# Kernel tuning notes

Hardware: AMD Instinct MI355X
Metric: run time of the kernel (lower is better)

## Reference

```python
import jax, jax.numpy as jnp
import numpy as np

N, E = 10000, 320000
IN_D, HID, OUT_D, EIN, KH = 128, 32, 128, 1, 32
BN_EPS = 1e-5  # torch BatchNorm1d default eps


def bn(x, g, b):
    # training-mode batch norm with biased variance (torch normalization semantics)
    m = jnp.mean(x, axis=0)
    v = jnp.mean((x - m) ** 2, axis=0)
    return g * (x - m) / jnp.sqrt(v + BN_EPS) + b


def setup_inputs() -> dict:
    key = jax.random.key(0)
    ks = jax.random.split(key, 8)

    def w(k, shape, s=0.05):
        return jax.random.normal(k, shape, dtype=jnp.float32) * s

    return {
        "H": jax.random.normal(ks[0], (N, IN_D), dtype=jnp.float32),
        "edge_attr": jax.random.normal(ks[1], (E, EIN), dtype=jnp.float32),
        "edges": jax.random.randint(ks[2], (2, E), 0, N),
        # linear1: input_dim -> hidden_dim
        "w1": w(ks[3], (HID, IN_D)), "b1": jnp.zeros((HID,), jnp.float32),
        # kernel MLP: edge_input_dim -> kernel_hidden -> (hidden+1)*hidden
        "kw1": w(ks[4], (KH, EIN)), "kb1": jnp.zeros((KH,), jnp.float32),
        "kw2": w(ks[5], ((HID + 1) * HID, KH)), "kb2": jnp.zeros(((HID + 1) * HID,), jnp.float32),
        # linear2: hidden -> output
        "w2": w(ks[6], (OUT_D, HID)), "b2": jnp.zeros((OUT_D,), jnp.float32),
        # batchnorm affine params
        "g_in": jnp.ones((IN_D,), jnp.float32), "beta_in": jnp.zeros((IN_D,), jnp.float32),
        "g_msg": jnp.ones((HID,), jnp.float32), "beta_msg": jnp.zeros((HID,), jnp.float32),
        "g_upd": jnp.ones((HID,), jnp.float32), "beta_upd": jnp.zeros((HID,), jnp.float32),
        "g_out": jnp.ones((OUT_D,), jnp.float32), "beta_out": jnp.zeros((OUT_D,), jnp.float32),
    }


def reference(H, edge_attr, edges, w1, b1, kw1, kb1, kw2, kb2, w2, b2,
              g_in, beta_in, g_msg, beta_msg, g_upd, beta_upd, g_out, beta_out):
    node_out, node_in = edges[0], edges[1]

    Hn = bn(H, g_in, beta_in)                    # input_batch_norm
    layer_input = jax.nn.relu(Hn)                # dropout -> identity (eval)

    # message: gather -> linear1 -> BN -> relu
    msg = layer_input[node_in] @ w1.T + b1       # [E, HID]
    msg = jax.nn.relu(bn(msg, g_msg, beta_msg))

    # edge-conditioned dynamic kernel: [E, HID+1, HID]
    kern = jax.nn.relu(edge_attr @ kw1.T + kb1) @ kw2.T + kb2
    kern = kern.reshape(E, HID + 1, HID)
    # per-edge matvec + per-edge bias row
    msg = jnp.einsum('ejk,ek->ej', kern[:, 1:, :], msg) + kern[:, 0, :]

    # aggregate: scatter_add into nodes
    upd = jax.ops.segment_sum(msg, node_out, num_segments=N)
    upd = jax.nn.relu(bn(upd, g_upd, beta_upd))

    out = upd @ w2.T + b2                        # linear2
    return bn(out, g_out, beta_out)              # output_batch_norm
```

## Files before the change

kernel.cpp:

```cpp
#include <hip/hip_runtime.h>
#include <math.h>

constexpr int N_    = 10000;
constexpr int E_    = 320000;
constexpr int IND   = 128;
constexpr int HID   = 32;
constexpr int OUTD  = 128;
constexpr int NIV   = 33;
constexpr float EPS = 1e-5f;

constexpr size_t OFF_SUMH   = 0;
constexpr size_t OFF_SQH    = 128;
constexpr size_t OFF_SUMP   = 256;
constexpr size_t OFF_SQP    = 288;
constexpr size_t OFF_SUMU   = 320;
constexpr size_t OFF_SQU    = 352;
constexpr size_t OFF_SUMO   = 384;
constexpr size_t OFF_SQO    = 512;
constexpr size_t OFF_OCC    = 640;
constexpr size_t OFF_DEGIN  = 704;
constexpr size_t OFF_DEGOUT = 10704;
constexpr size_t ZERO_CNT   = 20704;
constexpr size_t OFF_STARTS = 20740;
constexpr size_t OFF_CUR    = 30744;
constexpr size_t OFF_C1     = 40744;
constexpr size_t OFF_C0     = 75592;
constexpr size_t OFF_P      = 110440;
constexpr size_t OFF_UPD    = 430440;
constexpr size_t OFF_AEN    = 750440;

__device__ inline int compute_bps(const float* kw1, const float* kb1, float* bp) {
    int m = 0;
    for (int k = 0; k < 32; ++k) {
        float w = kw1[k];
        if (w != 0.f) bp[m++] = -kb1[k] / w;
    }
    for (int a = 1; a < m; ++a) {
        float v = bp[a]; int b = a - 1;
        while (b >= 0 && bp[b] > v) { bp[b+1] = bp[b]; --b; }
        bp[b+1] = v;
    }
    return m;
}

__global__ __launch_bounds__(256)
void k_A(const float* __restrict__ H,
         const float* __restrict__ ea, const int* __restrict__ edges,
         const float* __restrict__ kw1, const float* __restrict__ kb1,
         const float* __restrict__ kw2, const float* __restrict__ kb2,
         float* __restrict__ ws) {
    __shared__ float sel1[32], sel0[32];
    __shared__ float shS[256], shQ[256];
    __shared__ int locc[NIV];
    __shared__ float bps[32];
    int* wsi = (int*)ws;
    int t = threadIdx.x;
    int bid = blockIdx.x;

    if (bid < 33) {
        int i = bid;
        if (t == 0) {
            float bp[32];
            int m = compute_bps(kw1, kb1, bp);
            float arep;
            if (m == 0 || i > m) arep = 0.f;
            else if (i == 0)     arep = bp[0]   - (1.f + 0.5f*fabsf(bp[0]));
            else if (i == m)     arep = bp[m-1] + (1.f + 0.5f*fabsf(bp[m-1]));
            else                 arep = (bp[i-1] < bp[i]) ? 0.5f*(bp[i-1] + bp[i]) : bp[i-1];
            for (int k = 0; k < 32; ++k) {
                bool s = (arep * kw1[k] + kb1[k]) > 0.f;
                sel1[k] = s ? kw1[k] : 0.f;
                sel0[k] = s ? kb1[k] : 0.f;
            }
        }
        __syncthreads();
        for (int r = t; r < 1056; r += 256) {
            float a1 = 0.f, a0 = 0.f;
            for (int k = 0; k < 32; ++k) {
                float w = kw2[r*32 + k];
                a1 += w * sel1[k];
                a0 += w * sel0[k];
            }
            ws[OFF_C1 + (size_t)i*1056 + r] = a1;
            ws[OFF_C0 + (size_t)i*1056 + r] = a0 + kb2[r];
        }
    } else if (bid < 161) {
        int b2 = bid - 33;
        int col = t & 127, half = t >> 7;
        float s = 0.f, q = 0.f;
        for (int r = b2*2 + half; r < N_; r += 128*2) {
            float x = H[(size_t)r*IND + col];
            s += x; q += x*x;
        }
        shS[t] = s; shQ[t] = q;
        __syncthreads();
        if (t < 128) {
            atomicAdd(&ws[OFF_SUMH + t], shS[t] + shS[t+128]);
            atomicAdd(&ws[OFF_SQH  + t], shQ[t] + shQ[t+128]);
        }
    } else {
        int b2 = bid - 161;
        if (t < NIV) locc[t] = 0;
        if (t == 0) {
            float bp[32];
            int m = compute_bps(kw1, kb1, bp);
            for (int k = 0; k < 32; ++k) bps[k] = (k < m) ? bp[k] : 3.0e38f;
        }
        __syncthreads();
        for (int e = b2*256 + t; e < E_; e += 313*256) {
            float a = ea[e];
            int cnt = 0;
            #pragma unroll
            for (int k = 0; k < 32; ++k) cnt += (bps[k] < a) ? 1 : 0;
            atomicAdd(&locc[cnt], 1);
            atomicAdd(&wsi[OFF_DEGIN  + edges[E_ + e]], 1);
            atomicAdd(&wsi[OFF_DEGOUT + edges[e]],      1);
        }
        __syncthreads();
        if (t < NIV && locc[t] > 0) atomicAdd(&wsi[OFF_OCC + t], locc[t]);
    }
}

__global__ __launch_bounds__(256)
void k_B(const float* __restrict__ H, const float* __restrict__ w1,
         const float* __restrict__ b1, const float* __restrict__ g_in,
         const float* __restrict__ beta_in, float* __restrict__ ws) {
    __shared__ float w1L[32*129];
    __shared__ float xl[8][128];
    __shared__ int part[256];
    int* wsi = (int*)ws;
    int t = threadIdx.x;

    if (blockIdx.x == 0) {
        int base = t * 40;
        int loc[40];
        int s = 0;
        for (int i = 0; i < 40; ++i) {
            int idx = base + i;
            int v = (idx < N_) ? wsi[OFF_DEGOUT + idx] : 0;
            loc[i] = s; s += v;
        }
        part[t] = s;
        __syncthreads();
        for (int off = 1; off < 256; off <<= 1) {
            int add = (t >= off) ? part[t - off] : 0;
            __syncthreads();
            part[t] += add;
            __syncthreads();
        }
        int pre = (t > 0) ? part[t-1] : 0;
        for (int i = 0; i < 40; ++i) {
            int idx = base + i;
            if (idx <= N_) {
                int v = pre + loc[i];
                wsi[OFF_STARTS + idx] = v;
                if (idx < N_) wsi[OFF_CUR + idx] = v;
            }
        }
        return;
    }

    int g = t >> 5, j = t & 31;
    for (int idx = t; idx < 4096; idx += 256)
        w1L[(idx >> 7)*129 + (idx & 127)] = w1[idx];

    int n = (blockIdx.x - 1)*8 + g;
    float4 h4 = ((const float4*)(H + (size_t)n*IND))[j];
    float4 m4 = ((const float4*)(ws + OFF_SUMH))[j];
    float4 q4 = ((const float4*)(ws + OFF_SQH))[j];
    float4 gg = ((const float4*)g_in)[j];
    float4 bb = ((const float4*)beta_in)[j];
    float4 xv;
    {
        float* hp = (float*)&h4; float* mp = (float*)&m4; float* qp = (float*)&q4;
        float* gp = (float*)&gg; float* bp = (float*)&bb; float* xp = (float*)&xv;
        for (int i = 0; i < 4; ++i) {
            float mean = mp[i] * (1.f/N_);
            float var  = qp[i] * (1.f/N_) - mean*mean;
            float istd = 1.f / sqrtf(var + EPS);
            float gc = gp[i]*istd, bc = bp[i] - mean*gc;
            xp[i] = fmaxf(fmaf(gc, hp[i], bc), 0.f);
        }
    }
    ((float4*)&xl[g][0])[j] = xv;
    __syncthreads();
    float p = b1[j];
    const float* wr = &w1L[j*129];
    const float* xr = &xl[g][0];
    #pragma unroll 8
    for (int k = 0; k < 128; ++k) p = fmaf(wr[k], xr[k], p);
    ws[OFF_P + (size_t)n*HID + j] = p;
}

__global__ __launch_bounds__(256)
void k_C(const float* __restrict__ ea, const int* __restrict__ edges,
         const float* __restrict__ kw1, const float* __restrict__ kb1,
         float* __restrict__ ws) {
    __shared__ float shS[256], shQ[256];
    __shared__ float bps[32];
    int* wsi = (int*)ws;
    int t = threadIdx.x;
    if (blockIdx.x < 313) {
        if (t == 0) {
            float bp[32];
            int m = compute_bps(kw1, kb1, bp);
            for (int k = 0; k < 32; ++k) bps[k] = (k < m) ? bp[k] : 3.0e38f;
        }
        __syncthreads();
        float2* aen = (float2*)(ws + OFF_AEN);
        int b2 = blockIdx.x;
        for (int e = b2*256 + t; e < E_; e += 313*256) {
            int   nout = edges[e];
            int   nin  = edges[E_ + e];
            float a    = ea[e];
            int iv = 0;
            #pragma unroll
            for (int k = 0; k < 32; ++k) iv += (bps[k] < a) ? 1 : 0;
            int pos = atomicAdd(&wsi[OFF_CUR + nout], 1);
            float2 rec; rec.x = a; rec.y = __int_as_float(nin | (iv << 16));
            aen[pos] = rec;
        }
    } else {
        int b2 = blockIdx.x - 313;
        int j = t & 31, cp = t >> 5;
        float s = 0.f, q = 0.f;
        for (int n = b2*8 + cp; n < N_; n += 64*8) {
            float w = (float)wsi[OFF_DEGIN + n];
            float p = ws[OFF_P + (size_t)n*HID + j];
            s += w*p; q += w*p*p;
        }
        shS[t] = s; shQ[t] = q;
        __syncthreads();
        if (t < 32) {
            float S = 0.f, Qq = 0.f;
            for (int c = 0; c < 8; ++c) { S += shS[t + 32*c]; Qq += shQ[t + 32*c]; }
            atomicAdd(&ws[OFF_SUMP + t], S);
            atomicAdd(&ws[OFF_SQP  + t], Qq);
        }
    }
}

__global__ __launch_bounds__(256)
void k_D(const float* __restrict__ g_msg, const float* __restrict__ beta_msg,
         float* __restrict__ ws) {
    __shared__ float A[4][32*33];
    __shared__ float Bv[4][32];
    __shared__ float zl[8][4][32];
    __shared__ float shS[256], shQ[256];
    __shared__ int s_slot0, s_slot1;
    int* wsi = (int*)ws;
    int t = threadIdx.x, g = t >> 5, j = t & 31;

    if (t == 0) {
        int a0 = -1, a1 = -1;
        for (int i = 0; i < NIV; ++i)
            if (wsi[OFF_OCC + i] > 0) { if (a0 < 0) a0 = i; else if (a1 < 0) a1 = i; }
        s_slot0 = a0; s_slot1 = a1;
    }
    __syncthreads();
    int s0 = s_slot0, s1 = s_slot1;

    for (int idx = t; idx < 1024; idx += 256) {
        int jj = idx >> 5, kk = idx & 31;
        A[0][jj*33+kk] = (s0 >= 0) ? ws[OFF_C1 + (size_t)s0*1056 + 32 + idx] : 0.f;
        A[1][jj*33+kk] = (s0 >= 0) ? ws[OFF_C0 + (size_t)s0*1056 + 32 + idx] : 0.f;
        A[2][jj*33+kk] = (s1 >= 0) ? ws[OFF_C1 + (size_t)s1*1056 + 32 + idx] : 0.f;
        A[3][jj*33+kk] = (s1 >= 0) ? ws[OFF_C0 + (size_t)s1*1056 + 32 + idx] : 0.f;
    }
    if (t < 32) {
        Bv[0][t] = (s0 >= 0) ? ws[OFF_C1 + (size_t)s0*1056 + t] : 0.f;
        Bv[1][t] = (s0 >= 0) ? ws[OFF_C0 + (size_t)s0*1056 + t] : 0.f;
        Bv[2][t] = (s1 >= 0) ? ws[OFF_C1 + (size_t)s1*1056 + t] : 0.f;
        Bv[3][t] = (s1 >= 0) ? ws[OFF_C0 + (size_t)s1*1056 + t] : 0.f;
    }
    float mP = ws[OFF_SUMP + j] * (1.f/E_);
    float vP = ws[OFF_SQP  + j] * (1.f/E_) - mP*mP;
    float istd = 1.f / sqrtf(vP + EPS);
    float gc = g_msg[j]*istd, bc = beta_msg[j] - mP*gc;
    __syncthreads();

    int n = blockIdx.x*8 + g;
    int st = wsi[OFF_STARTS + n], en = wsi[OFF_STARTS + n + 1];
    float za0 = 0.f, zb0 = 0.f, za1 = 0.f, zb1 = 0.f;
    float suma0 = 0.f, suma1 = 0.f, c0f = 0.f, c1f = 0.f, rfall = 0.f;
    const float2* aen = (const float2*)(ws + OFF_AEN);

    for (int base = st; base < en; base += 32) {
        int cnt = en - base; if (cnt > 32) cnt = 32;
        float a_j = 0.f; int meta_j = 0;
        if (j < cnt) {
            float2 r = aen[base + j];
            a_j = r.x; meta_j = __float_as_int(r.y);
        }
        for (int k = 0; k < cnt; k += 4) {
            float pv[4], aa[4]; int ivv[4]; bool val[4];
            #pragma unroll
            for (int u = 0; u < 4; ++u) {
                int kk = (k + u) & 31;
                aa[u]  = __shfl(a_j, kk, 32);
                int mt = __shfl(meta_j, kk, 32);
                val[u] = (k + u) < cnt;
                int nin = mt & 0xFFFF; ivv[u] = mt >> 16;
                pv[u] = ws[OFF_P + (size_t)nin*HID + j];
            }
            #pragma unroll
            for (int u = 0; u < 4; ++u) {
                if (!val[u]) continue;
                float q = fmaxf(fmaf(gc, pv[u], bc), 0.f);
                float a = aa[u]; int iv = ivv[u];
                if (iv == s0)      { za0 = fmaf(a, q, za0); zb0 += q; suma0 += a; c0f += 1.f; }
                else if (iv == s1) { za1 = fmaf(a, q, za1); zb1 += q; suma1 += a; c1f += 1.f; }
                else {
                    const float* C1r = ws + OFF_C1 + (size_t)iv*1056;
                    const float* C0r = ws + OFF_C0 + (size_t)iv*1056;
                    float d1 = 0.f, d0 = 0.f;
                    for (int k2 = 0; k2 < 32; ++k2) {
                        float qk = __shfl(q, k2, 32);
                        d1 += C1r[32 + j*32 + k2] * qk;
                        d0 += C0r[32 + j*32 + k2] * qk;
                    }
                    rfall += a*(d1 + C1r[j]) + (d0 + C0r[j]);
                }
            }
        }
    }
    zl[g][0][j] = za0; zl[g][1][j] = zb0; zl[g][2][j] = za1; zl[g][3][j] = zb1;
    __syncthreads();

    float acc = rfall;
    if (s0 >= 0) acc += suma0*Bv[0][j] + c0f*Bv[1][j];
    if (s1 >= 0) acc += suma1*Bv[2][j] + c1f*Bv[3][j];
    const float* z0 = zl[g][0]; const float* z1 = zl[g][1];
    const float* z2 = zl[g][2]; const float* z3 = zl[g][3];
    #pragma unroll 4
    for (int k = 0; k < 32; ++k) {
        acc += A[0][j*33+k]*z0[k] + A[1][j*33+k]*z1[k]
             + A[2][j*33+k]*z2[k] + A[3][j*33+k]*z3[k];
    }
    ws[OFF_UPD + (size_t)n*HID + j] = acc;

    shS[t] = acc; shQ[t] = acc*acc;
    __syncthreads();
    if (t < 32) {
        float S = 0.f, Qq = 0.f;
        for (int c = 0; c < 8; ++c) { S += shS[t + 32*c]; Qq += shQ[t + 32*c]; }
        atomicAdd(&ws[OFF_SUMU + t], S);
        atomicAdd(&ws[OFF_SQU  + t], Qq);
    }
}

__global__ __launch_bounds__(256)
void k_F(const float* __restrict__ w2, const float* __restrict__ b2,
         const float* __restrict__ g_upd, const float* __restrict__ beta_upd,
         float* __restrict__ ws, float* __restrict__ out) {
    __shared__ float U[2][HID];
    __shared__ float shS[256], shQ[256];
    int t = threadIdx.x, nh = t >> 7, o = t & 127;
    float gc = 0.f, bc = 0.f;
    if (o < 32) {
        float m = ws[OFF_SUMU + o]*(1.f/N_);
        float v = ws[OFF_SQU  + o]*(1.f/N_) - m*m;
        float istd = 1.f/sqrtf(v + EPS);
        gc = g_upd[o]*istd; bc = beta_upd[o] - m*gc;
    }
    float w2r[32];
    for (int k = 0; k < 32; ++k) w2r[k] = w2[o*32 + k];
    float bo = b2[o];
    float sO = 0.f, qO = 0.f;
    for (int base = blockIdx.x*2; base < N_; base += gridDim.x*2) {
        int n = base + nh;
        if (o < 32) {
            float u = ws[OFF_UPD + (size_t)n*HID + o];
            U[nh][o] = fmaxf(fmaf(gc, u, bc), 0.f);
        }
        __syncthreads();
        float v = bo;
        for (int k = 0; k < 32; ++k) v = fmaf(w2r[k], U[nh][k], v);
        out[(size_t)n*OUTD + o] = v;
        sO += v; qO += v*v;
        __syncthreads();
    }
    shS[t] = sO; shQ[t] = qO;
    __syncthreads();
    if (t < 128) {
        atomicAdd(&ws[OFF_SUMO + t], shS[t] + shS[t+128]);
        atomicAdd(&ws[OFF_SQO  + t], shQ[t] + shQ[t+128]);
    }
}

__global__ __launch_bounds__(256)
void k_G(const float* __restrict__ g_out, const float* __restrict__ beta_out,
         const float* __restrict__ ws, float* __restrict__ out) {
    int g = blockIdx.x*blockDim.x + threadIdx.x;
    if (g >= N_*OUTD) return;
    int o = g & 127;
    float m = ws[OFF_SUMO + o]*(1.f/N_);
    float v = ws[OFF_SQO  + o]*(1.f/N_) - m*m;
    float istd = 1.f/sqrtf(v + EPS);
    out[g] = g_out[o]*istd*(out[g] - m) + beta_out[o];
}

extern "C" void kernel_launch(void* const* d_in, const int* in_sizes, int n_in,
                              void* d_out, int out_size, void* d_ws, size_t ws_size,
                              hipStream_t stream) {
    const float* H        = (const float*)d_in[0];
    const float* ea       = (const float*)d_in[1];
    const int*   edges    = (const int*)  d_in[2];
    const float* w1       = (const float*)d_in[3];
    const float* b1       = (const float*)d_in[4];
    const float* kw1      = (const float*)d_in[5];
    const float* kb1      = (const float*)d_in[6];
    const float* kw2      = (const float*)d_in[7];
    const float* kb2      = (const float*)d_in[8];
    const float* w2       = (const float*)d_in[9];
    const float* b2       = (const float*)d_in[10];
    const float* g_in     = (const float*)d_in[11];
    const float* beta_in  = (const float*)d_in[12];
    const float* g_msg    = (const float*)d_in[13];
    const float* beta_msg = (const float*)d_in[14];
    const float* g_upd    = (const float*)d_in[15];
    const float* beta_upd = (const float*)d_in[16];
    const float* g_out    = (const float*)d_in[17];
    const float* beta_out = (const float*)d_in[18];
    float* ws  = (float*)d_ws;
    float* out = (float*)d_out;

    hipMemsetAsync(d_ws, 0, ZERO_CNT*sizeof(float), stream);
    hipLaunchKernelGGL(k_A, dim3(474),  dim3(256), 0, stream, H, ea, edges, kw1, kb1, kw2, kb2, ws);
    hipLaunchKernelGGL(k_B, dim3(1251), dim3(256), 0, stream, H, w1, b1, g_in, beta_in, ws);
    hipLaunchKernelGGL(k_C, dim3(377),  dim3(256), 0, stream, ea, edges, kw1, kb1, ws);
    hipLaunchKernelGGL(k_D, dim3(1250), dim3(256), 0, stream, g_msg, beta_msg, ws);
    hipLaunchKernelGGL(k_F, dim3(250),  dim3(256), 0, stream, w2, b2, g_upd, beta_upd, ws, out);
    hipLaunchKernelGGL(k_G, dim3((N_*OUTD + 255)/256), dim3(256), 0, stream, g_out, beta_out, ws, out);
}
```

Measured before the change: 257.9 us.

## Map one node per wavefront in k_D with prefetched edge records

The aggregation kernel now gives each destination node a full 64-lane wavefront (4 nodes per block, twice the grid) instead of a 32-lane half-wave. Each lane loads the edge records itself, and the next 8 records are prefetched into registers while the current 8 are processed. Accumulation into the two dominant kernel slots becomes branchless masked FMAs, and the rare fallback path passes the q vector through shared memory instead of shuffles. This is meant to remove divergence between the two nodes that used to share a wave and to hide edge-record load latency. The cost is that the upper 32 lanes redo the lower half's work, so twice as many threads are used.

```diff
diff --git a/kernel.cpp b/kernel.cpp
--- a/kernel.cpp
+++ b/kernel.cpp
@@ -245,11 +245,15 @@
          float* __restrict__ ws) {
     __shared__ float A[4][32*33];
     __shared__ float Bv[4][32];
-    __shared__ float zl[8][4][32];
+    __shared__ float zx[4][4][32];
+    __shared__ float fb[4][32];
     __shared__ float shS[256], shQ[256];
     __shared__ int s_slot0, s_slot1;
     int* wsi = (int*)ws;
-    int t = threadIdx.x, g = t >> 5, j = t & 31;
+    int t = threadIdx.x;
+    int w = t >> 6;
+    int lane = t & 63;
+    int j = lane & 31;
 
     if (t == 0) {
         int a0 = -1, a1 = -1;
@@ -279,67 +283,81 @@
     float gc = g_msg[j]*istd, bc = beta_msg[j] - mP*gc;
     __syncthreads();
 
-    int n = blockIdx.x*8 + g;
+    int n = blockIdx.x*4 + w;
     int st = wsi[OFF_STARTS + n], en = wsi[OFF_STARTS + n + 1];
     float za0 = 0.f, zb0 = 0.f, za1 = 0.f, zb1 = 0.f;
     float suma0 = 0.f, suma1 = 0.f, c0f = 0.f, c1f = 0.f, rfall = 0.f;
     const float2* aen = (const float2*)(ws + OFF_AEN);
 
-    for (int base = st; base < en; base += 32) {
-        int cnt = en - base; if (cnt > 32) cnt = 32;
-        float a_j = 0.f; int meta_j = 0;
-        if (j < cnt) {
-            float2 r = aen[base + j];
-            a_j = r.x; meta_j = __float_as_int(r.y);
-        }
-        for (int k = 0; k < cnt; k += 4) {
-            float pv[4], aa[4]; int ivv[4]; bool val[4];
-            #pragma unroll
-            for (int u = 0; u < 4; ++u) {
-                int kk = (k + u) & 31;
-                aa[u]  = __shfl(a_j, kk, 32);
-                int mt = __shfl(meta_j, kk, 32);
-                val[u] = (k + u) < cnt;
-                int nin = mt & 0xFFFF; ivv[u] = mt >> 16;
-                pv[u] = ws[OFF_P + (size_t)nin*HID + j];
+    if (st < en) {
+        float2 rcur[8], rnext[8];
+        #pragma unroll
+        for (int q = 0; q < 8; ++q) {
+            int idx = st + q; if (idx >= en) idx = en - 1;
+            rcur[q] = aen[idx];
+        }
+        for (int base = st; base < en; base += 8) {
+            int nb = base + 8;
+            if (nb < en) {
+                #pragma unroll
+                for (int q = 0; q < 8; ++q) {
+                    int idx = nb + q; if (idx >= en) idx = en - 1;
+                    rnext[q] = aen[idx];
+                }
             }
             #pragma unroll
-            for (int u = 0; u < 4; ++u) {
-                if (!val[u]) continue;
-                float q = fmaxf(fmaf(gc, pv[u], bc), 0.f);
-                float a = aa[u]; int iv = ivv[u];
-                if (iv == s0)      { za0 = fmaf(a, q, za0); zb0 += q; suma0 += a; c0f += 1.f; }
-                else if (iv == s1) { za1 = fmaf(a, q, za1); zb1 += q; suma1 += a; c1f += 1.f; }
-                else {
+            for (int q = 0; q < 8; ++q) {
+                bool valid = (base + q) < en;
+                float a = rcur[q].x;
+                int  mt = __float_as_int(rcur[q].y);
+                int nin = mt & 0xFFFF, iv = mt >> 16;
+                float pv = ws[OFF_P + (size_t)nin*HID + j];
+                float qv = fmaxf(fmaf(gc, pv, bc), 0.f);
+                if (__builtin_expect(valid && iv != s0 && iv != s1, 0)) {
+                    if (lane < 32) fb[w][j] = qv;
                     const float* C1r = ws + OFF_C1 + (size_t)iv*1056;
                     const float* C0r = ws + OFF_C0 + (size_t)iv*1056;
                     float d1 = 0.f, d0 = 0.f;
                     for (int k2 = 0; k2 < 32; ++k2) {
-                        float qk = __shfl(q, k2, 32);
+                        float qk = fb[w][k2];
                         d1 += C1r[32 + j*32 + k2] * qk;
                         d0 += C0r[32 + j*32 + k2] * qk;
                     }
                     rfall += a*(d1 + C1r[j]) + (d0 + C0r[j]);
+                } else {
+                    float w0 = (valid && iv == s0) ? 1.f : 0.f;
+                    float w1 = (valid && iv == s1) ? 1.f : 0.f;
+                    float w0a = w0 * a, w1a = w1 * a;
+                    za0 = fmaf(w0a, qv, za0); zb0 = fmaf(w0, qv, zb0);
+                    za1 = fmaf(w1a, qv, za1); zb1 = fmaf(w1, qv, zb1);
+                    suma0 += w0a; c0f += w0;
+                    suma1 += w1a; c1f += w1;
                 }
             }
-        }
-    }
-    zl[g][0][j] = za0; zl[g][1][j] = zb0; zl[g][2][j] = za1; zl[g][3][j] = zb1;
+            #pragma unroll
+            for (int q = 0; q < 8; ++q) rcur[q] = rnext[q];
+        }
+    }
+
+    if (lane < 32) {
+        zx[w][0][j] = za0; zx[w][1][j] = zb0; zx[w][2][j] = za1; zx[w][3][j] = zb1;
+    }
     __syncthreads();
 
     float acc = rfall;
     if (s0 >= 0) acc += suma0*Bv[0][j] + c0f*Bv[1][j];
     if (s1 >= 0) acc += suma1*Bv[2][j] + c1f*Bv[3][j];
-    const float* z0 = zl[g][0]; const float* z1 = zl[g][1];
-    const float* z2 = zl[g][2]; const float* z3 = zl[g][3];
+    const float* z0 = zx[w][0]; const float* z1 = zx[w][1];
+    const float* z2 = zx[w][2]; const float* z3 = zx[w][3];
     #pragma unroll 4
     for (int k = 0; k < 32; ++k) {
         acc += A[0][j*33+k]*z0[k] + A[1][j*33+k]*z1[k]
              + A[2][j*33+k]*z2[k] + A[3][j*33+k]*z3[k];
     }
-    ws[OFF_UPD + (size_t)n*HID + j] = acc;
-
-    shS[t] = acc; shQ[t] = acc*acc;
+    if (lane < 32) ws[OFF_UPD + (size_t)n*HID + j] = acc;
+
+    shS[t] = (lane < 32) ? acc : 0.f;
+    shQ[t] = (lane < 32) ? acc*acc : 0.f;
     __syncthreads();
     if (t < 32) {
         float S = 0.f, Qq = 0.f;
@@ -429,7 +447,7 @@
     hipLaunchKernelGGL(k_A, dim3(474),  dim3(256), 0, stream, H, ea, edges, kw1, kb1, kw2, kb2, ws);
     hipLaunchKernelGGL(k_B, dim3(1251), dim3(256), 0, stream, H, w1, b1, g_in, beta_in, ws);
     hipLaunchKernelGGL(k_C, dim3(377),  dim3(256), 0, stream, ea, edges, kw1, kb1, ws);
-    hipLaunchKernelGGL(k_D, dim3(1250), dim3(256), 0, stream, g_msg, beta_msg, ws);
+    hipLaunchKernelGGL(k_D, dim3(2500), dim3(256), 0, stream, g_msg, beta_msg, ws);
     hipLaunchKernelGGL(k_F, dim3(250),  dim3(256), 0, stream, w2, b2, g_upd, beta_upd, ws, out);
     hipLaunchKernelGGL(k_G, dim3((N_*OUTD + 255)/256), dim3(256), 0, stream, g_out, beta_out, ws, out);
 }
```

Result: slower. 300.8 us (+16.6%).

## Fuse all stages into one cooperative persistent kernel with grid syncs

Applied to the files above, without the earlier changes.

Replaces the memset plus six kernel launches with a single cooperative kernel. It runs at most 512 persistent blocks and separates the stages with grid.sync, removing the per-launch gaps and drain bubbles between dependent kernels. The edge-aggregation inner loop is also unrolled to 8 and made branch-light by using predicated weights for the two common intervals. The prefix scan now recomputes degrees instead of keeping a per-thread local array. The cost is grid-wide barriers, fewer blocks than some stages previously used, and a fallback to the old multi-kernel path if the cooperative launch fails.

```diff
diff --git a/kernel.cpp b/kernel.cpp
--- a/kernel.cpp
+++ b/kernel.cpp
@@ -1,5 +1,8 @@
 #include <hip/hip_runtime.h>
+#include <hip/hip_cooperative_groups.h>
 #include <math.h>
+
+namespace cg = cooperative_groups;
 
 constexpr int N_    = 10000;
 constexpr int E_    = 320000;
@@ -44,6 +47,375 @@
 }
 
 __global__ __launch_bounds__(256)
+void k_mega(const float* __restrict__ H, const float* __restrict__ ea,
+            const int* __restrict__ edges,
+            const float* __restrict__ w1, const float* __restrict__ b1,
+            const float* __restrict__ kw1, const float* __restrict__ kb1,
+            const float* __restrict__ kw2, const float* __restrict__ kb2,
+            const float* __restrict__ w2, const float* __restrict__ b2,
+            const float* __restrict__ g_in, const float* __restrict__ beta_in,
+            const float* __restrict__ g_msg, const float* __restrict__ beta_msg,
+            const float* __restrict__ g_upd, const float* __restrict__ beta_upd,
+            const float* __restrict__ g_out, const float* __restrict__ beta_out,
+            float* __restrict__ ws, float* __restrict__ out) {
+    cg::grid_group grid = cg::this_grid();
+    __shared__ float S[6144];
+    __shared__ int s_slots[2];
+    int* wsi = (int*)ws;
+    const int t = threadIdx.x;
+    const int bid = blockIdx.x;
+    const int GD  = gridDim.x;
+
+    for (size_t i = (size_t)bid*256 + t; i < ZERO_CNT; i += (size_t)GD*256)
+        ws[i] = 0.f;
+    grid.sync();
+
+    {
+        float* sel1 = S;         float* sel0 = S + 32;
+        float* shS  = S + 64;    float* shQ  = S + 320;
+        int*   locc = (int*)(S + 576);
+        float* bps  = S + 640;
+        for (int task = bid; task < 474; task += GD) {
+            if (task < 33) {
+                int i = task;
+                if (t == 0) {
+                    float bp[32];
+                    int m = compute_bps(kw1, kb1, bp);
+                    float arep;
+                    if (m == 0 || i > m) arep = 0.f;
+                    else if (i == 0)     arep = bp[0]   - (1.f + 0.5f*fabsf(bp[0]));
+                    else if (i == m)     arep = bp[m-1] + (1.f + 0.5f*fabsf(bp[m-1]));
+                    else                 arep = (bp[i-1] < bp[i]) ? 0.5f*(bp[i-1] + bp[i]) : bp[i-1];
+                    for (int k = 0; k < 32; ++k) {
+                        bool s = (arep * kw1[k] + kb1[k]) > 0.f;
+                        sel1[k] = s ? kw1[k] : 0.f;
+                        sel0[k] = s ? kb1[k] : 0.f;
+                    }
+                }
+                __syncthreads();
+                for (int r = t; r < 1056; r += 256) {
+                    float a1 = 0.f, a0 = 0.f;
+                    for (int k = 0; k < 32; ++k) {
+                        float w = kw2[r*32 + k];
+                        a1 += w * sel1[k];
+                        a0 += w * sel0[k];
+                    }
+                    ws[OFF_C1 + (size_t)i*1056 + r] = a1;
+                    ws[OFF_C0 + (size_t)i*1056 + r] = a0 + kb2[r];
+                }
+            } else if (task < 161) {
+                int b2 = task - 33;
+                int col = t & 127, half = t >> 7;
+                float s = 0.f, q = 0.f;
+                for (int r = b2*2 + half; r < N_; r += 128*2) {
+                    float x = H[(size_t)r*IND + col];
+                    s += x; q += x*x;
+                }
+                shS[t] = s; shQ[t] = q;
+                __syncthreads();
+                if (t < 128) {
+                    atomicAdd(&ws[OFF_SUMH + t], shS[t] + shS[t+128]);
+                    atomicAdd(&ws[OFF_SQH  + t], shQ[t] + shQ[t+128]);
+                }
+            } else {
+                int b2 = task - 161;
+                if (t < NIV) locc[t] = 0;
+                if (t == 0) {
+                    float bp[32];
+                    int m = compute_bps(kw1, kb1, bp);
+                    for (int k = 0; k < 32; ++k) bps[k] = (k < m) ? bp[k] : 3.0e38f;
+                }
+                __syncthreads();
+                for (int e = b2*256 + t; e < E_; e += 313*256) {
+                    float a = ea[e];
+                    int cnt = 0;
+                    #pragma unroll
+                    for (int k = 0; k < 32; ++k) cnt += (bps[k] < a) ? 1 : 0;
+                    atomicAdd(&locc[cnt], 1);
+                    atomicAdd(&wsi[OFF_DEGIN  + edges[E_ + e]], 1);
+                    atomicAdd(&wsi[OFF_DEGOUT + edges[e]],      1);
+                }
+                __syncthreads();
+                if (t < NIV && locc[t] > 0) atomicAdd(&wsi[OFF_OCC + t], locc[t]);
+            }
+            __syncthreads();
+        }
+    }
+    grid.sync();
+
+    {
+        float* w1L  = S;
+        float* xl   = S + 4128;
+        int*   part = (int*)(S + 5152);
+        for (int idx = t; idx < 4096; idx += 256)
+            w1L[(idx >> 7)*129 + (idx & 127)] = w1[idx];
+        __syncthreads();
+        for (int task = bid; task < 1251; task += GD) {
+            if (task == 0) {
+                int base = t * 40;
+                int s = 0;
+                for (int i = 0; i < 40; ++i) {
+                    int idx = base + i;
+                    s += (idx < N_) ? wsi[OFF_DEGOUT + idx] : 0;
+                }
+                part[t] = s;
+                __syncthreads();
+                for (int off = 1; off < 256; off <<= 1) {
+                    int add = (t >= off) ? part[t - off] : 0;
+                    __syncthreads();
+                    part[t] += add;
+                    __syncthreads();
+                }
+                int run = (t > 0) ? part[t-1] : 0;
+                for (int i = 0; i < 40; ++i) {
+                    int idx = base + i;
+                    if (idx <= N_) {
+                        wsi[OFF_STARTS + idx] = run;
+                        if (idx < N_) {
+                            wsi[OFF_CUR + idx] = run;
+                            run += wsi[OFF_DEGOUT + idx];
+                        }
+                    }
+                }
+            } else {
+                int g = t >> 5, j = t & 31;
+                int n = (task - 1)*8 + g;
+                float* xlg = xl + g*128;
+                float4 h4 = ((const float4*)(H + (size_t)n*IND))[j];
+                float4 m4 = ((const float4*)(ws + OFF_SUMH))[j];
+                float4 q4 = ((const float4*)(ws + OFF_SQH))[j];
+                float4 gg = ((const float4*)g_in)[j];
+                float4 bb = ((const float4*)beta_in)[j];
+                float4 xv;
+                {
+                    float* hp = (float*)&h4; float* mp = (float*)&m4; float* qp = (float*)&q4;
+                    float* gp = (float*)&gg; float* bp = (float*)&bb; float* xp = (float*)&xv;
+                    for (int i = 0; i < 4; ++i) {
+                        float mean = mp[i] * (1.f/N_);
+                        float var  = qp[i] * (1.f/N_) - mean*mean;
+                        float istd = 1.f / sqrtf(var + EPS);
+                        float gcv = gp[i]*istd, bcv = bp[i] - mean*gcv;
+                        xp[i] = fmaxf(fmaf(gcv, hp[i], bcv), 0.f);
+                    }
+                }
+                ((float4*)xlg)[j] = xv;
+                __syncthreads();
+                float p = b1[j];
+                const float* wr = &w1L[j*129];
+                #pragma unroll 8
+                for (int k = 0; k < 128; ++k) p = fmaf(wr[k], xlg[k], p);
+                ws[OFF_P + (size_t)n*HID + j] = p;
+            }
+            __syncthreads();
+        }
+    }
+    grid.sync();
+
+    {
+        float* bps = S;
+        float* shS = S + 64;  float* shQ = S + 320;
+        for (int task = bid; task < 377; task += GD) {
+            if (task < 313) {
+                if (t == 0) {
+                    float bp[32];
+                    int m = compute_bps(kw1, kb1, bp);
+                    for (int k = 0; k < 32; ++k) bps[k] = (k < m) ? bp[k] : 3.0e38f;
+                }
+                __syncthreads();
+                float2* aen = (float2*)(ws + OFF_AEN);
+                for (int e = task*256 + t; e < E_; e += 313*256) {
+                    int   nout = edges[e];
+                    int   nin  = edges[E_ + e];
+                    float a    = ea[e];
+                    int iv = 0;
+                    #pragma unroll
+                    for (int k = 0; k < 32; ++k) iv += (bps[k] < a) ? 1 : 0;
+                    int pos = atomicAdd(&wsi[OFF_CUR + nout], 1);
+                    float2 rec; rec.x = a; rec.y = __int_as_float(nin | (iv << 16));
+                    aen[pos] = rec;
+                }
+            } else {
+                int b2 = task - 313;
+                int j = t & 31, cp = t >> 5;
+                float s = 0.f, q = 0.f;
+                for (int n = b2*8 + cp; n < N_; n += 64*8) {
+                    float w = (float)wsi[OFF_DEGIN + n];
+                    float p = ws[OFF_P + (size_t)n*HID + j];
+                    s += w*p; q += w*p*p;
+                }
+                shS[t] = s; shQ[t] = q;
+                __syncthreads();
+                if (t < 32) {
+                    float Sm = 0.f, Qq = 0.f;
+                    for (int c = 0; c < 8; ++c) { Sm += shS[t + 32*c]; Qq += shQ[t + 32*c]; }
+                    atomicAdd(&ws[OFF_SUMP + t], Sm);
+                    atomicAdd(&ws[OFF_SQP  + t], Qq);
+                }
+            }
+            __syncthreads();
+        }
+    }
+    grid.sync();
+
+    {
+        float* A   = S;
+        float* Bv  = S + 4224;
+        float* zl  = S + 4352;
+        float* shS = S + 5376;   float* shQ = S + 5632;
+        int g = t >> 5, j = t & 31;
+        if (t == 0) {
+            int a0 = -1, a1 = -1;
+            for (int i = 0; i < NIV; ++i)
+                if (wsi[OFF_OCC + i] > 0) { if (a0 < 0) a0 = i; else if (a1 < 0) a1 = i; }
+            s_slots[0] = a0; s_slots[1] = a1;
+        }
+        __syncthreads();
+        int s0 = s_slots[0], s1 = s_slots[1];
+        for (int idx = t; idx < 1024; idx += 256) {
+            int jj = idx >> 5, kk = idx & 31;
+            A[0*1056 + jj*33+kk] = (s0 >= 0) ? ws[OFF_C1 + (size_t)s0*1056 + 32 + idx] : 0.f;
+            A[1*1056 + jj*33+kk] = (s0 >= 0) ? ws[OFF_C0 + (size_t)s0*1056 + 32 + idx] : 0.f;
+            A[2*1056 + jj*33+kk] = (s1 >= 0) ? ws[OFF_C1 + (size_t)s1*1056 + 32 + idx] : 0.f;
+            A[3*1056 + jj*33+kk] = (s1 >= 0) ? ws[OFF_C0 + (size_t)s1*1056 + 32 + idx] : 0.f;
+        }
+        if (t < 32) {
+            Bv[0*32+t] = (s0 >= 0) ? ws[OFF_C1 + (size_t)s0*1056 + t] : 0.f;
+            Bv[1*32+t] = (s0 >= 0) ? ws[OFF_C0 + (size_t)s0*1056 + t] : 0.f;
+            Bv[2*32+t] = (s1 >= 0) ? ws[OFF_C1 + (size_t)s1*1056 + t] : 0.f;
+            Bv[3*32+t] = (s1 >= 0) ? ws[OFF_C0 + (size_t)s1*1056 + t] : 0.f;
+        }
+        float mP = ws[OFF_SUMP + j] * (1.f/E_);
+        float vP = ws[OFF_SQP  + j] * (1.f/E_) - mP*mP;
+        float istd = 1.f / sqrtf(vP + EPS);
+        float gc = g_msg[j]*istd, bc = beta_msg[j] - mP*gc;
+        __syncthreads();
+
+        float sumS = 0.f, sumQ = 0.f;
+        const float2* aen = (const float2*)(ws + OFF_AEN);
+        for (int task = bid; task < 1250; task += GD) {
+            int n = task*8 + g;
+            int st = wsi[OFF_STARTS + n], en = wsi[OFF_STARTS + n + 1];
+            float za0 = 0.f, zb0 = 0.f, za1 = 0.f, zb1 = 0.f;
+            float suma0 = 0.f, suma1 = 0.f, c0f = 0.f, c1f = 0.f, rfall = 0.f;
+            for (int base = st; base < en; base += 32) {
+                int cnt = en - base; if (cnt > 32) cnt = 32;
+                float a_j = 0.f; int meta_j = 0;
+                if (j < cnt) {
+                    float2 r = aen[base + j];
+                    a_j = r.x; meta_j = __float_as_int(r.y);
+                }
+                for (int k = 0; k < cnt; k += 8) {
+                    float pv[8], aa[8]; int ivv[8]; bool val[8];
+                    #pragma unroll
+                    for (int u = 0; u < 8; ++u) {
+                        int kk = (k + u) & 31;
+                        aa[u]  = __shfl(a_j, kk, 32);
+                        int mt = __shfl(meta_j, kk, 32);
+                        val[u] = (k + u) < cnt;
+                        int nin = mt & 0xFFFF; ivv[u] = mt >> 16;
+                        pv[u] = ws[OFF_P + (size_t)nin*HID + j];
+                    }
+                    #pragma unroll
+                    for (int u = 0; u < 8; ++u) {
+                        float qv = fmaxf(fmaf(gc, pv[u], bc), 0.f);
+                        float a = aa[u]; int iv = ivv[u];
+                        if (__builtin_expect(val[u] && iv != s0 && iv != s1, 0)) {
+                            const float* C1r = ws + OFF_C1 + (size_t)iv*1056;
+                            const float* C0r = ws + OFF_C0 + (size_t)iv*1056;
+                            float d1 = 0.f, d0 = 0.f;
+                            for (int k2 = 0; k2 < 32; ++k2) {
+                                float qk = __shfl(qv, k2, 32);
+                                d1 += C1r[32 + j*32 + k2] * qk;
+                                d0 += C0r[32 + j*32 + k2] * qk;
+                            }
+                            rfall += a*(d1 + C1r[j]) + (d0 + C0r[j]);
+                        } else {
+                            float w0 = (val[u] && iv == s0) ? 1.f : 0.f;
+                            float w1v = (val[u] && iv == s1) ? 1.f : 0.f;
+                            float w0a = w0 * a, w1a = w1v * a;
+                            za0 = fmaf(w0a, qv, za0); zb0 = fmaf(w0, qv, zb0);
+                            za1 = fmaf(w1a, qv, za1); zb1 = fmaf(w1v, qv, zb1);
+                            suma0 += w0a; c0f += w0;
+                            suma1 += w1a; c1f += w1v;
+                        }
+                    }
+                }
+            }
+            zl[(g*4+0)*32+j] = za0; zl[(g*4+1)*32+j] = zb0;
+            zl[(g*4+2)*32+j] = za1; zl[(g*4+3)*32+j] = zb1;
+            __syncthreads();
+            float acc = rfall;
+            if (s0 >= 0) acc += suma0*Bv[0*32+j] + c0f*Bv[1*32+j];
+            if (s1 >= 0) acc += suma1*Bv[2*32+j] + c1f*Bv[3*32+j];
+            const float* z0 = zl + (g*4+0)*32; const float* z1 = zl + (g*4+1)*32;
+            const float* z2 = zl + (g*4+2)*32; const float* z3 = zl + (g*4+3)*32;
+            #pragma unroll 4
+            for (int k = 0; k < 32; ++k) {
+                acc += A[0*1056 + j*33+k]*z0[k] + A[1*1056 + j*33+k]*z1[k]
+                     + A[2*1056 + j*33+k]*z2[k] + A[3*1056 + j*33+k]*z3[k];
+            }
+            ws[OFF_UPD + (size_t)n*HID + j] = acc;
+            sumS += acc; sumQ += acc*acc;
+            __syncthreads();
+        }
+        shS[t] = sumS; shQ[t] = sumQ;
+        __syncthreads();
+        if (t < 32) {
+            float Sm = 0.f, Qq = 0.f;
+            for (int c = 0; c < 8; ++c) { Sm += shS[t + 32*c]; Qq += shQ[t + 32*c]; }
+            atomicAdd(&ws[OFF_SUMU + t], Sm);
+            atomicAdd(&ws[OFF_SQU  + t], Qq);
+        }
+    }
+    grid.sync();
+
+    {
+        float* U   = S;
+        float* shS = S + 64;   float* shQ = S + 320;
+        int nh = t >> 7, o = t & 127;
+        float gc = 0.f, bc = 0.f;
+        if (o < 32) {
+            float m = ws[OFF_SUMU + o]*(1.f/N_);
+            float v = ws[OFF_SQU  + o]*(1.f/N_) - m*m;
+            float istd = 1.f/sqrtf(v + EPS);
+            gc = g_upd[o]*istd; bc = beta_upd[o] - m*gc;
+        }
+        float w2r[32];
+        for (int k = 0; k < 32; ++k) w2r[k] = w2[o*32 + k];
+        float bo = b2[o];
+        float sO = 0.f, qO = 0.f;
+        for (int task = bid; task < 5000; task += GD) {
+            int n = task*2 + nh;
+            if (o < 32) {
+                float u = ws[OFF_UPD + (size_t)n*HID + o];
+                U[nh*32 + o] = fmaxf(fmaf(gc, u, bc), 0.f);
+            }
+            __syncthreads();
+            float v = bo;
+            for (int k = 0; k < 32; ++k) v = fmaf(w2r[k], U[nh*32 + k], v);
+            out[(size_t)n*OUTD + o] = v;
+            sO += v; qO += v*v;
+            __syncthreads();
+        }
+        shS[t] = sO; shQ[t] = qO;
+        __syncthreads();
+        if (t < 128) {
+            atomicAdd(&ws[OFF_SUMO + t], shS[t] + shS[t+128]);
+            atomicAdd(&ws[OFF_SQO  + t], shQ[t] + shQ[t+128]);
+        }
+    }
+    grid.sync();
+
+    for (size_t i = (size_t)bid*256 + t; i < (size_t)N_*OUTD; i += (size_t)GD*256) {
+        int o = (int)(i & 127);
+        float m = ws[OFF_SUMO + o]*(1.f/N_);
+        float v = ws[OFF_SQO  + o]*(1.f/N_) - m*m;
+        float istd = 1.f/sqrtf(v + EPS);
+        out[i] = g_out[o]*istd*(out[i] - m) + beta_out[o];
+    }
+}
+
+__global__ __launch_bounds__(256)
 void k_A(const float* __restrict__ H,
          const float* __restrict__ ea, const int* __restrict__ edges,
          const float* __restrict__ kw1, const float* __restrict__ kb1,
@@ -56,7 +428,6 @@
     int* wsi = (int*)ws;
     int t = threadIdx.x;
     int bid = blockIdx.x;
-
     if (bid < 33) {
         int i = bid;
         if (t == 0) {
@@ -130,15 +501,12 @@
     __shared__ int part[256];
     int* wsi = (int*)ws;
     int t = threadIdx.x;
-
     if (blockIdx.x == 0) {
         int base = t * 40;
-        int loc[40];
         int s = 0;
         for (int i = 0; i < 40; ++i) {
             int idx = base + i;
-            int v = (idx < N_) ? wsi[OFF_DEGOUT + idx] : 0;
-            loc[i] = s; s += v;
+            s += (idx < N_) ? wsi[OFF_DEGOUT + idx] : 0;
         }
         part[t] = s;
         __syncthreads();
@@ -148,22 +516,19 @@
             part[t] += add;
             __syncthreads();
         }
-        int pre = (t > 0) ? part[t-1] : 0;
+        int run = (t > 0) ? part[t-1] : 0;
         for (int i = 0; i < 40; ++i) {
             int idx = base + i;
             if (idx <= N_) {
-                int v = pre + loc[i];
-                wsi[OFF_STARTS + idx] = v;
-                if (idx < N_) wsi[OFF_CUR + idx] = v;
+                wsi[OFF_STARTS + idx] = run;
+                if (idx < N_) { wsi[OFF_CUR + idx] = run; run += wsi[OFF_DEGOUT + idx]; }
             }
         }
         return;
     }
-
     int g = t >> 5, j = t & 31;
     for (int idx = t; idx < 4096; idx += 256)
         w1L[(idx >> 7)*129 + (idx & 127)] = w1[idx];
-
     int n = (blockIdx.x - 1)*8 + g;
     float4 h4 = ((const float4*)(H + (size_t)n*IND))[j];
     float4 m4 = ((const float4*)(ws + OFF_SUMH))[j];
@@ -250,7 +615,6 @@
     __shared__ int s_slot0, s_slot1;
     int* wsi = (int*)ws;
     int t = threadIdx.x, g = t >> 5, j = t & 31;
-
     if (t == 0) {
         int a0 = -1, a1 = -1;
         for (int i = 0; i < NIV; ++i)
@@ -259,7 +623,6 @@
     }
     __syncthreads();
     int s0 = s_slot0, s1 = s_slot1;
-
     for (int idx = t; idx < 1024; idx += 256) {
         int jj = idx >> 5, kk = idx & 31;
         A[0][jj*33+kk] = (s0 >= 0) ? ws[OFF_C1 + (size_t)s0*1056 + 32 + idx] : 0.f;
@@ -278,13 +641,11 @@
     float istd = 1.f / sqrtf(vP + EPS);
     float gc = g_msg[j]*istd, bc = beta_msg[j] - mP*gc;
     __syncthreads();
-
     int n = blockIdx.x*8 + g;
     int st = wsi[OFF_STARTS + n], en = wsi[OFF_STARTS + n + 1];
     float za0 = 0.f, zb0 = 0.f, za1 = 0.f, zb1 = 0.f;
     float suma0 = 0.f, suma1 = 0.f, c0f = 0.f, c1f = 0.f, rfall = 0.f;
     const float2* aen = (const float2*)(ws + OFF_AEN);
-
     for (int base = st; base < en; base += 32) {
         int cnt = en - base; if (cnt > 32) cnt = 32;
         float a_j = 0.f; int meta_j = 0;
@@ -292,10 +653,10 @@
             float2 r = aen[base + j];
             a_j = r.x; meta_j = __float_as_int(r.y);
         }
-        for (int k = 0; k < cnt; k += 4) {
-            float pv[4], aa[4]; int ivv[4]; bool val[4];
+        for (int k = 0; k < cnt; k += 8) {
+            float pv[8], aa[8]; int ivv[8]; bool val[8];
             #pragma unroll
-            for (int u = 0; u < 4; ++u) {
+            for (int u = 0; u < 8; ++u) {
                 int kk = (k + u) & 31;
                 aa[u]  = __shfl(a_j, kk, 32);
                 int mt = __shfl(meta_j, kk, 32);
@@ -304,29 +665,33 @@
                 pv[u] = ws[OFF_P + (size_t)nin*HID + j];
             }
             #pragma unroll
-            for (int u = 0; u < 4; ++u) {
-                if (!val[u]) continue;
-                float q = fmaxf(fmaf(gc, pv[u], bc), 0.f);
+            for (int u = 0; u < 8; ++u) {
+                float qv = fmaxf(fmaf(gc, pv[u], bc), 0.f);
                 float a = aa[u]; int iv = ivv[u];
-                if (iv == s0)      { za0 = fmaf(a, q, za0); zb0 += q; suma0 += a; c0f += 1.f; }
-                else if (iv == s1) { za1 = fmaf(a, q, za1); zb1 += q; suma1 += a; c1f += 1.f; }
-                else {
+                if (__builtin_expect(val[u] && iv != s0 && iv != s1, 0)) {
                     const float* C1r = ws + OFF_C1 + (size_t)iv*1056;
                     const float* C0r = ws + OFF_C0 + (size_t)iv*1056;
                     float d1 = 0.f, d0 = 0.f;
                     for (int k2 = 0; k2 < 32; ++k2) {
-                        float qk = __shfl(q, k2, 32);
+                        float qk = __shfl(qv, k2, 32);
                         d1 += C1r[32 + j*32 + k2] * qk;
                         d0 += C0r[32 + j*32 + k2] * qk;
                     }
                     rfall += a*(d1 + C1r[j]) + (d0 + C0r[j]);
+                } else {
+                    float w0 = (val[u] && iv == s0) ? 1.f : 0.f;
+                    float w1v = (val[u] && iv == s1) ? 1.f : 0.f;
+                    float w0a = w0 * a, w1a = w1v * a;
+                    za0 = fmaf(w0a, qv, za0); zb0 = fmaf(w0, qv, zb0);
+                    za1 = fmaf(w1a, qv, za1); zb1 = fmaf(w1v, qv, zb1);
+                    suma0 += w0a; c0f += w0;
+                    suma1 += w1a; c1f += w1v;
                 }
             }
         }
     }
     zl[g][0][j] = za0; zl[g][1][j] = zb0; zl[g][2][j] = za1; zl[g][3][j] = zb1;
     __syncthreads();
-
     float acc = rfall;
     if (s0 >= 0) acc += suma0*Bv[0][j] + c0f*Bv[1][j];
     if (s1 >= 0) acc += suma1*Bv[2][j] + c1f*Bv[3][j];
@@ -338,7 +703,6 @@
              + A[2][j*33+k]*z2[k] + A[3][j*33+k]*z3[k];
     }
     ws[OFF_UPD + (size_t)n*HID + j] = acc;
-
     shS[t] = acc; shQ[t] = acc*acc;
     __syncthreads();
     if (t < 32) {
@@ -425,11 +789,30 @@
     float* ws  = (float*)d_ws;
     float* out = (float*)d_out;
 
-    hipMemsetAsync(d_ws, 0, ZERO_CNT*sizeof(float), stream);
-    hipLaunchKernelGGL(k_A, dim3(474),  dim3(256), 0, stream, H, ea, edges, kw1, kb1, kw2, kb2, ws);
-    hipLaunchKernelGGL(k_B, dim3(1251), dim3(256), 0, stream, H, w1, b1, g_in, beta_in, ws);
-    hipLaunchKernelGGL(k_C, dim3(377),  dim3(256), 0, stream, ea, edges, kw1, kb1, ws);
-    hipLaunchKernelGGL(k_D, dim3(1250), dim3(256), 0, stream, g_msg, beta_msg, ws);
-    hipLaunchKernelGGL(k_F, dim3(250),  dim3(256), 0, stream, w2, b2, g_upd, beta_upd, ws, out);
-    hipLaunchKernelGGL(k_G, dim3((N_*OUTD + 255)/256), dim3(256), 0, stream, g_out, beta_out, ws, out);
+    int perCU = 0;
+    hipError_t oerr = hipOccupancyMaxActiveBlocksPerMultiprocessor(&perCU, k_mega, 256, 0);
+    int blocks = (oerr == hipSuccess && perCU > 0) ? perCU * 256 : 0;
+    if (blocks > 512) blocks = 512;
+
+    hipError_t lerr = hipErrorUnknown;
+    if (blocks > 0) {
+        void* args[] = {
+            (void*)&H, (void*)&ea, (void*)&edges, (void*)&w1, (void*)&b1,
+            (void*)&kw1, (void*)&kb1, (void*)&kw2, (void*)&kb2,
+            (void*)&w2, (void*)&b2, (void*)&g_in, (void*)&beta_in,
+            (void*)&g_msg, (void*)&beta_msg, (void*)&g_upd, (void*)&beta_upd,
+            (void*)&g_out, (void*)&beta_out, (void*)&ws, (void*)&out
+        };
+        lerr = hipLaunchCooperativeKernel((void*)k_mega, dim3(blocks), dim3(256),
+                                          args, 0, stream);
+    }
+    if (lerr != hipSuccess) {
+        hipMemsetAsync(d_ws, 0, ZERO_CNT*sizeof(float), stream);
+        hipLaunchKernelGGL(k_A, dim3(474),  dim3(256), 0, stream, H, ea, edges, kw1, kb1, kw2, kb2, ws);
+        hipLaunchKernelGGL(k_B, dim3(1251), dim3(256), 0, stream, H, w1, b1, g_in, beta_in, ws);
+        hipLaunchKernelGGL(k_C, dim3(377),  dim3(256), 0, stream, ea, edges, kw1, kb1, ws);
+        hipLaunchKernelGGL(k_D, dim3(1250), dim3(256), 0, stream, g_msg, beta_msg, ws);
+        hipLaunchKernelGGL(k_F, dim3(250),  dim3(256), 0, stream, w2, b2, g_upd, beta_upd, ws, out);
+        hipLaunchKernelGGL(k_G, dim3((N_*OUTD + 255)/256), dim3(256), 0, stream, g_out, beta_out, ws, out);
+    }
 }
```

Measured after the change: 462.6 us. 1.79x slower.

## Flatten k_D edge loop across warps for 20-node blocks with shared-memory atomics

Applied to the files above, without the earlier changes.

k_D now has each block own 20 consecutive destination nodes and spreads all their edges across the 8 warps, instead of one warp walking one node's edge list. The local node index is packed into the edge record; the source index and interval id are repacked into fewer bits. Per-node partial sums are accumulated with LDS float atomics, then finished with float4 reads from a padded coefficient tile. The aim is to even out per-node degree imbalance and raise memory-level parallelism, at the cost of shared atomics and fewer blocks.

```diff
diff --git a/kernel.cpp b/kernel.cpp
--- a/kernel.cpp
+++ b/kernel.cpp
@@ -7,6 +7,7 @@
 constexpr int HID   = 32;
 constexpr int OUTD  = 128;
 constexpr int NIV   = 33;
+constexpr int NPB   = 20;
 constexpr float EPS = 1e-5f;
 
 constexpr size_t OFF_SUMH   = 0;
@@ -216,8 +217,10 @@
             int iv = 0;
             #pragma unroll
             for (int k = 0; k < 32; ++k) iv += (bps[k] < a) ? 1 : 0;
+            int nl = nout % NPB;
             int pos = atomicAdd(&wsi[OFF_CUR + nout], 1);
-            float2 rec; rec.x = a; rec.y = __int_as_float(nin | (iv << 16));
+            float2 rec; rec.x = a;
+            rec.y = __int_as_float(nin | (iv << 14) | (nl << 20));
             aen[pos] = rec;
         }
     } else {
@@ -243,11 +246,13 @@
 __global__ __launch_bounds__(256)
 void k_D(const float* __restrict__ g_msg, const float* __restrict__ beta_msg,
          float* __restrict__ ws) {
-    __shared__ float A[4][32*33];
+    __shared__ __align__(16) float A[4][32*36];
     __shared__ float Bv[4][32];
-    __shared__ float zl[8][4][32];
+    __shared__ __align__(16) float accZ[NPB][4][32];
+    __shared__ float accS[NPB][4];
+    __shared__ float accF[NPB][32];
     __shared__ float shS[256], shQ[256];
-    __shared__ int s_slot0, s_slot1;
+    __shared__ int s_slots[2];
     int* wsi = (int*)ws;
     int t = threadIdx.x, g = t >> 5, j = t & 31;
 
@@ -255,17 +260,20 @@
         int a0 = -1, a1 = -1;
         for (int i = 0; i < NIV; ++i)
             if (wsi[OFF_OCC + i] > 0) { if (a0 < 0) a0 = i; else if (a1 < 0) a1 = i; }
-        s_slot0 = a0; s_slot1 = a1;
-    }
-    __syncthreads();
-    int s0 = s_slot0, s1 = s_slot1;
+        s_slots[0] = a0; s_slots[1] = a1;
+    }
+    for (int idx = t; idx < NPB*4*32; idx += 256) ((float*)accZ)[idx] = 0.f;
+    for (int idx = t; idx < NPB*4;    idx += 256) ((float*)accS)[idx] = 0.f;
+    for (int idx = t; idx < NPB*32;   idx += 256) ((float*)accF)[idx] = 0.f;
+    __syncthreads();
+    int s0 = s_slots[0], s1 = s_slots[1];
 
     for (int idx = t; idx < 1024; idx += 256) {
         int jj = idx >> 5, kk = idx & 31;
-        A[0][jj*33+kk] = (s0 >= 0) ? ws[OFF_C1 + (size_t)s0*1056 + 32 + idx] : 0.f;
-        A[1][jj*33+kk] = (s0 >= 0) ? ws[OFF_C0 + (size_t)s0*1056 + 32 + idx] : 0.f;
-        A[2][jj*33+kk] = (s1 >= 0) ? ws[OFF_C1 + (size_t)s1*1056 + 32 + idx] : 0.f;
-        A[3][jj*33+kk] = (s1 >= 0) ? ws[OFF_C0 + (size_t)s1*1056 + 32 + idx] : 0.f;
+        A[0][jj*36+kk] = (s0 >= 0) ? ws[OFF_C1 + (size_t)s0*1056 + 32 + idx] : 0.f;
+        A[1][jj*36+kk] = (s0 >= 0) ? ws[OFF_C0 + (size_t)s0*1056 + 32 + idx] : 0.f;
+        A[2][jj*36+kk] = (s1 >= 0) ? ws[OFF_C1 + (size_t)s1*1056 + 32 + idx] : 0.f;
+        A[3][jj*36+kk] = (s1 >= 0) ? ws[OFF_C0 + (size_t)s1*1056 + 32 + idx] : 0.f;
     }
     if (t < 32) {
         Bv[0][t] = (s0 >= 0) ? ws[OFF_C1 + (size_t)s0*1056 + t] : 0.f;
@@ -279,67 +287,83 @@
     float gc = g_msg[j]*istd, bc = beta_msg[j] - mP*gc;
     __syncthreads();
 
-    int n = blockIdx.x*8 + g;
-    int st = wsi[OFF_STARTS + n], en = wsi[OFF_STARTS + n + 1];
-    float za0 = 0.f, zb0 = 0.f, za1 = 0.f, zb1 = 0.f;
-    float suma0 = 0.f, suma1 = 0.f, c0f = 0.f, c1f = 0.f, rfall = 0.f;
+    int n0 = blockIdx.x * NPB;
+    int span0 = wsi[OFF_STARTS + n0], span1 = wsi[OFF_STARTS + n0 + NPB];
     const float2* aen = (const float2*)(ws + OFF_AEN);
 
-    for (int base = st; base < en; base += 32) {
-        int cnt = en - base; if (cnt > 32) cnt = 32;
-        float a_j = 0.f; int meta_j = 0;
-        if (j < cnt) {
-            float2 r = aen[base + j];
-            a_j = r.x; meta_j = __float_as_int(r.y);
-        }
-        for (int k = 0; k < cnt; k += 4) {
-            float pv[4], aa[4]; int ivv[4]; bool val[4];
+    for (int e0 = span0 + g; e0 < span1; e0 += 32) {
+        float2 rc[4]; bool v[4]; float pv[4]; int mt[4];
+        #pragma unroll
+        for (int u = 0; u < 4; ++u) {
+            int e = e0 + 8*u;
+            v[u] = e < span1;
+            rc[u] = v[u] ? aen[e] : make_float2(0.f, __int_as_float(0));
+        }
+        #pragma unroll
+        for (int u = 0; u < 4; ++u) {
+            mt[u] = __float_as_int(rc[u].y);
+            pv[u] = ws[OFF_P + (size_t)(mt[u] & 0x3FFF)*HID + j];
+        }
+        #pragma unroll
+        for (int u = 0; u < 4; ++u) {
+            if (!v[u]) continue;
+            float a  = rc[u].x;
+            int   iv = (mt[u] >> 14) & 0x3F;
+            int   nl = mt[u] >> 20;
+            float qv = fmaxf(fmaf(gc, pv[u], bc), 0.f);
+            if (iv == s0) {
+                atomicAdd(&accZ[nl][0][j], a*qv);
+                atomicAdd(&accZ[nl][1][j], qv);
+                if (j == 0) { atomicAdd(&accS[nl][0], a); atomicAdd(&accS[nl][1], 1.f); }
+            } else if (iv == s1) {
+                atomicAdd(&accZ[nl][2][j], a*qv);
+                atomicAdd(&accZ[nl][3][j], qv);
+                if (j == 0) { atomicAdd(&accS[nl][2], a); atomicAdd(&accS[nl][3], 1.f); }
+            } else {
+                const float* C1r = ws + OFF_C1 + (size_t)iv*1056;
+                const float* C0r = ws + OFF_C0 + (size_t)iv*1056;
+                float d1 = 0.f, d0 = 0.f;
+                for (int k2 = 0; k2 < 32; ++k2) {
+                    float qk = __shfl(qv, (g & 1)*32 + k2, 64);
+                    d1 += C1r[32 + j*32 + k2] * qk;
+                    d0 += C0r[32 + j*32 + k2] * qk;
+                }
+                atomicAdd(&accF[nl][j], a*(d1 + C1r[j]) + (d0 + C0r[j]));
+            }
+        }
+    }
+    __syncthreads();
+
+    float sumS = 0.f, sumQ = 0.f;
+    for (int r = 0; r < NPB; r += 8) {
+        int nl = r + g;
+        if (nl < NPB) {
+            float acc = accF[nl][j];
+            float sa0 = accS[nl][0], c0 = accS[nl][1];
+            float sa1 = accS[nl][2], c1 = accS[nl][3];
+            if (s0 >= 0) acc += sa0*Bv[0][j] + c0*Bv[1][j];
+            if (s1 >= 0) acc += sa1*Bv[2][j] + c1*Bv[3][j];
             #pragma unroll
-            for (int u = 0; u < 4; ++u) {
-                int kk = (k + u) & 31;
-                aa[u]  = __shfl(a_j, kk, 32);
-                int mt = __shfl(meta_j, kk, 32);
-                val[u] = (k + u) < cnt;
-                int nin = mt & 0xFFFF; ivv[u] = mt >> 16;
-                pv[u] = ws[OFF_P + (size_t)nin*HID + j];
+            for (int k4 = 0; k4 < 8; ++k4) {
+                float4 z0 = *(const float4*)&accZ[nl][0][k4*4];
+                float4 z1 = *(const float4*)&accZ[nl][1][k4*4];
+                float4 z2 = *(const float4*)&accZ[nl][2][k4*4];
+                float4 z3 = *(const float4*)&accZ[nl][3][k4*4];
+                float4 a0 = *(const float4*)&A[0][j*36 + k4*4];
+                float4 a1 = *(const float4*)&A[1][j*36 + k4*4];
+                float4 a2 = *(const float4*)&A[2][j*36 + k4*4];
+                float4 a3 = *(const float4*)&A[3][j*36 + k4*4];
+                acc += a0.x*z0.x + a0.y*z0.y + a0.z*z0.z + a0.w*z0.w
+                     + a1.x*z1.x + a1.y*z1.y + a1.z*z1.z + a1.w*z1.w
+                     + a2.x*z2.x + a2.y*z2.y + a2.z*z2.z + a2.w*z2.w
+                     + a3.x*z3.x + a3.y*z3.y + a3.z*z3.z + a3.w*z3.w;
             }
-            #pragma unroll
-            for (int u = 0; u < 4; ++u) {
-                if (!val[u]) continue;
-                float q = fmaxf(fmaf(gc, pv[u], bc), 0.f);
-                float a = aa[u]; int iv = ivv[u];
-                if (iv == s0)      { za0 = fmaf(a, q, za0); zb0 += q; suma0 += a; c0f += 1.f; }
-                else if (iv == s1) { za1 = fmaf(a, q, za1); zb1 += q; suma1 += a; c1f += 1.f; }
-                else {
-                    const float* C1r = ws + OFF_C1 + (size_t)iv*1056;
-                    const float* C0r = ws + OFF_C0 + (size_t)iv*1056;
-                    float d1 = 0.f, d0 = 0.f;
-                    for (int k2 = 0; k2 < 32; ++k2) {
-                        float qk = __shfl(q, k2, 32);
-                        d1 += C1r[32 + j*32 + k2] * qk;
-                        d0 += C0r[32 + j*32 + k2] * qk;
-                    }
-                    rfall += a*(d1 + C1r[j]) + (d0 + C0r[j]);
-                }
-            }
-        }
-    }
-    zl[g][0][j] = za0; zl[g][1][j] = zb0; zl[g][2][j] = za1; zl[g][3][j] = zb1;
-    __syncthreads();
-
-    float acc = rfall;
-    if (s0 >= 0) acc += suma0*Bv[0][j] + c0f*Bv[1][j];
-    if (s1 >= 0) acc += suma1*Bv[2][j] + c1f*Bv[3][j];
-    const float* z0 = zl[g][0]; const float* z1 = zl[g][1];
-    const float* z2 = zl[g][2]; const float* z3 = zl[g][3];
-    #pragma unroll 4
-    for (int k = 0; k < 32; ++k) {
-        acc += A[0][j*33+k]*z0[k] + A[1][j*33+k]*z1[k]
-             + A[2][j*33+k]*z2[k] + A[3][j*33+k]*z3[k];
-    }
-    ws[OFF_UPD + (size_t)n*HID + j] = acc;
-
-    shS[t] = acc; shQ[t] = acc*acc;
+            int n = n0 + nl;
+            ws[OFF_UPD + (size_t)n*HID + j] = acc;
+            sumS += acc; sumQ += acc*acc;
+        }
+    }
+    shS[t] = sumS; shQ[t] = sumQ;
     __syncthreads();
     if (t < 32) {
         float S = 0.f, Qq = 0.f;
@@ -429,7 +453,7 @@
     hipLaunchKernelGGL(k_A, dim3(474),  dim3(256), 0, stream, H, ea, edges, kw1, kb1, kw2, kb2, ws);
     hipLaunchKernelGGL(k_B, dim3(1251), dim3(256), 0, stream, H, w1, b1, g_in, beta_in, ws);
     hipLaunchKernelGGL(k_C, dim3(377),  dim3(256), 0, stream, ea, edges, kw1, kb1, ws);
-    hipLaunchKernelGGL(k_D, dim3(1250), dim3(256), 0, stream, g_msg, beta_msg, ws);
+    hipLaunchKernelGGL(k_D, dim3(N_/NPB), dim3(256), 0, stream, g_msg, beta_msg, ws);
     hipLaunchKernelGGL(k_F, dim3(250),  dim3(256), 0, stream, w2, b2, g_upd, beta_upd, ws, out);
     hipLaunchKernelGGL(k_G, dim3((N_*OUTD + 255)/256), dim3(256), 0, stream, g_out, beta_out, ws, out);
 }
```

Result: slower. 340.4 us (+32.0%).
